# Kernel tuning notes

Measured on AMD Instinct MI355X. Metric: run time of the kernel, lower is better.

Reference implementation:

```python
import jax, jax.numpy as jnp
import numpy as np

HEADS = 8
HEAD_DIM = 64
INV_TEMP = HEAD_DIM ** -0.5
LN_EPS = 1e-5  # torch nn.LayerNorm default


def layer_norm(x, g, b):
    mu = jnp.mean(x, axis=-1, keepdims=True)
    var = jnp.var(x, axis=-1, keepdims=True)
    return (x - mu) * jax.lax.rsqrt(var + LN_EPS) * g + b


def setup_inputs() -> dict:
    key = jax.random.key(0)
    ks = jax.random.split(key, 10)
    B, P, N, C = 2, 64, 256, 512
    std = C ** -0.5
    return {
        "q": jax.random.normal(ks[0], (B, P, N, C), jnp.float32),
        "k": jax.random.normal(ks[1], (B, P, N, C), jnp.float32),
        "v": jax.random.normal(ks[2], (B, P, N, C), jnp.float32),
        "mask": jax.random.uniform(ks[3], (B, P, 1, N, N), jnp.float32),
        "pos_scores": jax.random.normal(ks[4], (1, 1, HEADS, N, N), jnp.float32),
        "ln_q_g": jnp.ones((C,), jnp.float32), "ln_q_b": jnp.zeros((C,), jnp.float32),
        "ln_k_g": jnp.ones((C,), jnp.float32), "ln_k_b": jnp.zeros((C,), jnp.float32),
        "ln_v_g": jnp.ones((C,), jnp.float32), "ln_v_b": jnp.zeros((C,), jnp.float32),
        "Wq": jax.random.normal(ks[5], (C, C), jnp.float32) * std,
        "Wk": jax.random.normal(ks[6], (C, C), jnp.float32) * std,
        "Wv": jax.random.normal(ks[7], (C, C), jnp.float32) * std,
        "Wo": jax.random.normal(ks[8], (C, C), jnp.float32) * std,
        "bo": jnp.zeros((C,), jnp.float32),
    }


def reference(q, k, v, mask, pos_scores, ln_q_g, ln_q_b, ln_k_g, ln_k_b,
              ln_v_g, ln_v_b, Wq, Wk, Wv, Wo, bo):
    B, P, N, C = q.shape
    # pre-norm + projections (nn.Linear: y = x @ W^T)
    qh = jnp.einsum('bpnc,ec->bpne', layer_norm(q, ln_q_g, ln_q_b), Wq)
    kh = jnp.einsum('bpnc,ec->bpne', layer_norm(k, ln_k_g, ln_k_b), Wk)
    vh = jnp.einsum('bpnc,ec->bpne', layer_norm(v, ln_v_g, ln_v_b), Wv)
    # split heads: b p n (h d) -> b p h n d
    split = lambda t: t.reshape(B, P, N, HEADS, HEAD_DIM).transpose(0, 1, 3, 2, 4)
    qh, kh, vh = split(qh), split(kh), split(vh)
    # windowed attention with additive pos bias and multiplicative mask
    sim = jnp.einsum('bphid,bphjd->bphij', qh, kh) * INV_TEMP
    sim = mask * (sim + pos_scores)
    attn = jax.nn.softmax(sim, axis=-1)
    out = jnp.einsum('bphij,bphjd->bphid', attn, vh)
    # merge heads: b p h n d -> b p n (h d)
    out = out.transpose(0, 1, 3, 2, 4).reshape(B, P, N, C)
    return jnp.einsum('bpnc,ec->bpne', out, Wo) + bo
```

## Files before the change

### kernel.cpp

```cpp
#include <hip/hip_runtime.h>
#include <hip/hip_fp16.h>

#define BP   128
#define NTOK 256
#define CDIM 512
#define ROWS 32768
#define NH   8
#define DH   64

typedef _Float16 h2_t __attribute__((ext_vector_type(2)));
typedef _Float16 h4_t __attribute__((ext_vector_type(4)));
typedef _Float16 h8_t __attribute__((ext_vector_type(8)));
typedef float    f4_t __attribute__((ext_vector_type(4)));
typedef unsigned int u2v __attribute__((ext_vector_type(2)));

__device__ __forceinline__ unsigned pkrtz(float a, float b) {
    return __builtin_bit_cast(unsigned, __builtin_amdgcn_cvt_pkrtz(a, b));
}

__device__ __forceinline__ void async16(const void* gptr, void* lptr) {
    __builtin_amdgcn_global_load_lds(
        (const __attribute__((address_space(1))) unsigned int*)gptr,
        (__attribute__((address_space(3))) unsigned int*)lptr, 16, 0, 0);
}

__device__ __forceinline__ u2v pl32swap(unsigned a, unsigned b) {
#if __has_builtin(__builtin_amdgcn_permlane32_swap)
    return __builtin_amdgcn_permlane32_swap(a, b, false, false);
#else
    const bool hi = (threadIdx.x & 32) != 0;
    unsigned sa = (unsigned)__shfl_xor((int)a, 32);
    unsigned sb = (unsigned)__shfl_xor((int)b, 32);
    u2v r; r[0] = hi ? sb : a; r[1] = hi ? b : sa; return r;
#endif
}

__device__ __forceinline__ u2v pl16swap(unsigned a, unsigned b) {
#if __has_builtin(__builtin_amdgcn_permlane16_swap)
    return __builtin_amdgcn_permlane16_swap(a, b, false, false);
#else
    const bool odd = (threadIdx.x & 16) != 0;
    unsigned sa = (unsigned)__shfl_xor((int)a, 16);
    unsigned sb = (unsigned)__shfl_xor((int)b, 16);
    u2v r; r[0] = odd ? sb : a; r[1] = odd ? b : sa; return r;
#endif
}

__global__ __launch_bounds__(256) void ln_cast(const float* __restrict__ x,
                                               const float* __restrict__ g,
                                               const float* __restrict__ b,
                                               _Float16* __restrict__ y) {
    const int wave = threadIdx.x >> 6, lane = threadIdx.x & 63;
    const size_t row = (size_t)blockIdx.x * 4 + wave;
    const float4* xr = (const float4*)(x + row * CDIM);
    float4 a0 = xr[2 * lane], a1 = xr[2 * lane + 1];
    float s  = a0.x + a0.y + a0.z + a0.w + a1.x + a1.y + a1.z + a1.w;
    float ss = a0.x * a0.x + a0.y * a0.y + a0.z * a0.z + a0.w * a0.w +
               a1.x * a1.x + a1.y * a1.y + a1.z * a1.z + a1.w * a1.w;
#pragma unroll
    for (int off = 32; off; off >>= 1) {
        s  += __shfl_xor(s, off);
        ss += __shfl_xor(ss, off);
    }
    const float mu = s * (1.f / 512.f);
    const float rs = rsqrtf(ss * (1.f / 512.f) - mu * mu + 1e-5f);
    const float4* gp = (const float4*)g;
    const float4* bpp = (const float4*)b;
    float4 g0 = gp[2 * lane], g1 = gp[2 * lane + 1];
    float4 b0 = bpp[2 * lane], b1 = bpp[2 * lane + 1];
    h8_t o;
    o[0] = (_Float16)((a0.x - mu) * rs * g0.x + b0.x);
    o[1] = (_Float16)((a0.y - mu) * rs * g0.y + b0.y);
    o[2] = (_Float16)((a0.z - mu) * rs * g0.z + b0.z);
    o[3] = (_Float16)((a0.w - mu) * rs * g0.w + b0.w);
    o[4] = (_Float16)((a1.x - mu) * rs * g1.x + b1.x);
    o[5] = (_Float16)((a1.y - mu) * rs * g1.y + b1.y);
    o[6] = (_Float16)((a1.z - mu) * rs * g1.z + b1.z);
    o[7] = (_Float16)((a1.w - mu) * rs * g1.w + b1.w);
    ((h8_t*)(y + row * CDIM))[lane] = o;
}

__global__ __launch_bounds__(256) void cast_w4(const float* __restrict__ w0,
                                               const float* __restrict__ w1,
                                               const float* __restrict__ w2,
                                               const float* __restrict__ w3,
                                               _Float16* __restrict__ o) {
    const float* srcs[4] = {w0, w1, w2, w3};
    const float* w = srcs[blockIdx.y];
    const float scale = (blockIdx.y == 0) ? 0.125f : 1.0f;
    _Float16* dst = o + (size_t)blockIdx.y * (CDIM * CDIM);
    const int idx = blockIdx.x * 256 + threadIdx.x;
    float4 v = ((const float4*)w)[idx];
    h4_t ov = {(_Float16)(v.x * scale), (_Float16)(v.y * scale),
               (_Float16)(v.z * scale), (_Float16)(v.w * scale)};
    ((h4_t*)dst)[idx] = ov;
}

template <int MODE>
__global__ __launch_bounds__(256) void gemm_bt(const _Float16* __restrict__ A,
                                               const _Float16* __restrict__ Bw,
                                               _Float16* __restrict__ Ch,
                                               float* __restrict__ Cf,
                                               const float* __restrict__ bias) {
    constexpr int K = CDIM;
    __shared__ __align__(16) _Float16 As[128 * 64];
    __shared__ __align__(16) _Float16 Bs[128 * 64];
    const int t = threadIdx.x;
    const int wave = t >> 6, lane = t & 63;
    const int wm = wave & 1, wn = wave >> 1;

    const int bid = blockIdx.x;
    const int xcd = bid & 7, idx = bid >> 3;
    const size_t rowBase = (size_t)(xcd * 32 + (idx >> 2)) * 128;
    const int colBase = (idx & 3) * 128;

    f4_t acc[4][4] = {};

    const int srow = t >> 3;
    const int scol = (t & 7) * 8;
    const _Float16* Ap = A + (rowBase + srow) * K + scol;
    const _Float16* Bp = Bw + ((size_t)colBase + srow) * K + scol;
    char* AsB = (char*)As + wave * 1024;
    char* BsB = (char*)Bs + wave * 1024;

    for (int k0 = 0; k0 < K; k0 += 64) {
#pragma unroll
        for (int c = 0; c < 4; ++c) {
            async16(Ap + (size_t)(32 * c) * K + k0, AsB + c * 4096);
            async16(Bp + (size_t)(32 * c) * K + k0, BsB + c * 4096);
        }
        __syncthreads();
#pragma unroll
        for (int kk = 0; kk < 64; kk += 32) {
            h8_t af[4], bf[4];
#pragma unroll
            for (int i = 0; i < 4; ++i)
                af[i] = *(const h8_t*)(As + (wm * 64 + i * 16 + (lane & 15)) * 64 +
                                       kk + (lane >> 4) * 8);
#pragma unroll
            for (int j = 0; j < 4; ++j)
                bf[j] = *(const h8_t*)(Bs + (wn * 64 + j * 16 + (lane & 15)) * 64 +
                                       kk + (lane >> 4) * 8);
#pragma unroll
            for (int i = 0; i < 4; ++i)
#pragma unroll
                for (int j = 0; j < 4; ++j)
                    acc[i][j] = __builtin_amdgcn_mfma_f32_16x16x32_f16(
                        af[i], bf[j], acc[i][j], 0, 0, 0);
        }
        __syncthreads();
    }
#pragma unroll
    for (int i = 0; i < 4; ++i) {
        const size_t growb = rowBase + wm * 64 + i * 16 + ((lane >> 4) * 4);
#pragma unroll
        for (int j = 0; j < 4; ++j) {
            const int gcol = colBase + wn * 64 + j * 16 + (lane & 15);
            if (MODE == 2) {
                const int bp = (int)(growb >> 8), tok = (int)(growb & 255);
                const int hh = gcol >> 6, dd = gcol & 63;
                h4_t w = {(_Float16)acc[i][j][0], (_Float16)acc[i][j][1],
                          (_Float16)acc[i][j][2], (_Float16)acc[i][j][3]};
                *(h4_t*)(Ch + ((size_t)(bp * NH + hh) * DH + dd) * NTOK + tok) = w;
            } else {
#pragma unroll
                for (int r = 0; r < 4; ++r) {
                    const size_t idx2 = (growb + r) * CDIM + gcol;
                    if (MODE == 0)
                        Ch[idx2] = (_Float16)acc[i][j][r];
                    else
                        Cf[idx2] = acc[i][j][r] + bias[gcol];
                }
            }
        }
    }
}

__global__ __launch_bounds__(256, 2) void attn_mfma(const _Float16* __restrict__ Q,
                                                    const _Float16* __restrict__ K,
                                                    const _Float16* __restrict__ VT,
                                                    const float* __restrict__ mask,
                                                    const float* __restrict__ pos,
                                                    _Float16* __restrict__ O) {
    const int bid = blockIdx.x;
    const int xcd = bid & 7, idx = bid >> 3;
    const int bp = xcd + 8 * (idx >> 4);
    const int sub = idx & 15;
    const int h = sub & 7, qh = sub >> 3;

    const int t = threadIdx.x;
    const int wave = t >> 6, lane = t & 63;
    const int g = lane >> 4, li = lane & 15;

    __shared__ __align__(16) _Float16 Ks[2][64 * 64];
    __shared__ __align__(16) _Float16 VTs[2][64 * 64];

    const int i0 = qh * 128 + wave * 32;

    h8_t qf[2][2];
#pragma unroll
    for (int it = 0; it < 2; ++it)
#pragma unroll
        for (int x = 0; x < 2; ++x)
            qf[it][x] = *(const h8_t*)(Q +
                (size_t)(bp * NTOK + i0 + it * 16 + li) * CDIM +
                h * DH + x * 32 + g * 8);

    const int srow = wave * 16 + (lane >> 3);
    const int sslot = (lane & 7) ^ ((lane >> 3) & 7);
    const _Float16* kSrc = K + ((size_t)(bp * NTOK) + srow) * CDIM + h * DH + sslot * 8;
    const _Float16* vSrc = VT + ((size_t)((bp * NH + h) * DH) + srow) * NTOK + sslot * 8;
    char* KsB[2] = {(char*)Ks[0] + wave * 2048, (char*)Ks[1] + wave * 2048};
    char* VsB[2] = {(char*)VTs[0] + wave * 2048, (char*)VTs[1] + wave * 2048};

    const int sw = li & 7;
    const int cx0 = (g ^ sw) * 8;
    const int cx1 = ((4 + g) ^ sw) * 8;

    const float* mrow0 = mask + (size_t)bp * (NTOK * NTOK) + (size_t)(i0 + li) * NTOK + g * 4;
    const float* prow0 = pos + (size_t)h * (NTOK * NTOK) + (size_t)(i0 + li) * NTOK + g * 4;

    f4_t o[4][2] = {};
    float lp[2] = {0.f, 0.f};

    async16(kSrc, KsB[0]);
    async16(kSrc + 8 * CDIM, KsB[0] + 1024);
    async16(vSrc, VsB[0]);
    async16(vSrc + 8 * NTOK, VsB[0] + 1024);

#pragma unroll
    for (int c = 0; c < 4; ++c) {
        const int cur = c & 1;
        if (c < 3) {
            const int nb = cur ^ 1;
            async16(kSrc + (size_t)(c + 1) * 64 * CDIM, KsB[nb]);
            async16(kSrc + (size_t)(c + 1) * 64 * CDIM + 8 * CDIM, KsB[nb] + 1024);
            async16(vSrc + (c + 1) * 64, VsB[nb]);
            async16(vSrc + (c + 1) * 64 + 8 * NTOK, VsB[nb] + 1024);
            asm volatile("s_waitcnt vmcnt(4)" ::: "memory");
        } else {
            asm volatile("s_waitcnt vmcnt(0)" ::: "memory");
        }
        __builtin_amdgcn_s_barrier();
        __builtin_amdgcn_sched_barrier(0);

        const _Float16* Kc = Ks[cur];
        const _Float16* Vc = VTs[cur];

        f4_t s[4][2] = {};
#pragma unroll
        for (int x = 0; x < 2; ++x) {
            const int cc = x ? cx1 : cx0;
            h8_t kf[4];
#pragma unroll
            for (int jt = 0; jt < 4; ++jt)
                kf[jt] = *(const h8_t*)(Kc + (jt * 16 + li) * 64 + cc);
#pragma unroll
            for (int jt = 0; jt < 4; ++jt)
#pragma unroll
                for (int it = 0; it < 2; ++it)
                    s[jt][it] = __builtin_amdgcn_mfma_f32_16x16x32_f16(
                        kf[jt], qf[it][x], s[jt][it], 0, 0, 0);
        }

        h8_t pf[2][2];
#pragma unroll
        for (int it = 0; it < 2; ++it) {
            const float* mr = mrow0 + it * (16 * NTOK) + c * 64;
            const float* pr = prow0 + it * (16 * NTOK) + c * 64;
            unsigned pk[4][2];
#pragma unroll
            for (int jt = 0; jt < 4; ++jt) {
                float4 mm = *(const float4*)(mr + jt * 16);
                float4 pp = *(const float4*)(pr + jt * 16);
                float e0 = __expf((s[jt][it][0] + pp.x) * mm.x);
                float e1 = __expf((s[jt][it][1] + pp.y) * mm.y);
                float e2 = __expf((s[jt][it][2] + pp.z) * mm.z);
                float e3 = __expf((s[jt][it][3] + pp.w) * mm.w);
                lp[it] += (e0 + e1) + (e2 + e3);
                pk[jt][0] = pkrtz(e0, e1);
                pk[jt][1] = pkrtz(e2, e3);
            }
#pragma unroll
            for (int x = 0; x < 2; ++x) {
                u2v r0 = pl32swap(pk[2 * x][0], pk[2 * x + 1][0]);
                u2v r1 = pl32swap(pk[2 * x][1], pk[2 * x + 1][1]);
                u2v q0 = pl16swap(r0[0], r0[1]);
                u2v q1 = pl16swap(r1[0], r1[1]);
                union { unsigned u[4]; h8_t v; } u;
                u.u[0] = q0[0]; u.u[1] = q1[0]; u.u[2] = q0[1]; u.u[3] = q1[1];
                pf[it][x] = u.v;
            }
        }

#pragma unroll
        for (int x = 0; x < 2; ++x) {
            const int cc = x ? cx1 : cx0;
            h8_t vf[4];
#pragma unroll
            for (int dt = 0; dt < 4; ++dt)
                vf[dt] = *(const h8_t*)(Vc + (dt * 16 + li) * 64 + cc);
#pragma unroll
            for (int dt = 0; dt < 4; ++dt)
#pragma unroll
                for (int it = 0; it < 2; ++it)
                    o[dt][it] = __builtin_amdgcn_mfma_f32_16x16x32_f16(
                        vf[dt], pf[it][x], o[dt][it], 0, 0, 0);
        }
        __builtin_amdgcn_sched_barrier(0);
        __builtin_amdgcn_s_barrier();
    }

    float inv[2];
#pragma unroll
    for (int it = 0; it < 2; ++it) {
        float l = lp[it];
        l += __shfl_xor(l, 16);
        l += __shfl_xor(l, 32);
        inv[it] = __builtin_amdgcn_rcpf(l);
    }
#pragma unroll
    for (int dt = 0; dt < 4; ++dt)
#pragma unroll
        for (int it = 0; it < 2; ++it) {
            const int i = i0 + it * 16 + li;
            h4_t w = {(_Float16)(o[dt][it][0] * inv[it]),
                      (_Float16)(o[dt][it][1] * inv[it]),
                      (_Float16)(o[dt][it][2] * inv[it]),
                      (_Float16)(o[dt][it][3] * inv[it])};
            *(h4_t*)(O + (size_t)(bp * NTOK + i) * CDIM + h * DH + dt * 16 +
                     g * 4) = w;
        }
}

extern "C" void kernel_launch(void* const* d_in, const int* in_sizes, int n_in,
                              void* d_out, int out_size, void* d_ws, size_t ws_size,
                              hipStream_t stream) {
    const float* q    = (const float*)d_in[0];
    const float* k    = (const float*)d_in[1];
    const float* v    = (const float*)d_in[2];
    const float* mask = (const float*)d_in[3];
    const float* pos  = (const float*)d_in[4];
    const float* lnqg = (const float*)d_in[5];
    const float* lnqb = (const float*)d_in[6];
    const float* lnkg = (const float*)d_in[7];
    const float* lnkb = (const float*)d_in[8];
    const float* lnvg = (const float*)d_in[9];
    const float* lnvb = (const float*)d_in[10];
    const float* Wq   = (const float*)d_in[11];
    const float* Wk   = (const float*)d_in[12];
    const float* Wv   = (const float*)d_in[13];
    const float* Wo   = (const float*)d_in[14];
    const float* bo   = (const float*)d_in[15];
    float* out = (float*)d_out;

    char* ws = (char*)d_ws;
    const size_t XSZ = (size_t)ROWS * CDIM * sizeof(_Float16);
    _Float16* XB  = (_Float16*)ws;
    _Float16* WH  = (_Float16*)(ws + XSZ);
    _Float16* QHp = (_Float16*)(ws + XSZ + 4 * (size_t)(CDIM * CDIM) * sizeof(_Float16));
    _Float16* KHp = QHp + (size_t)ROWS * CDIM;
    _Float16* VTg = KHp + (size_t)ROWS * CDIM;

    cast_w4<<<dim3(256, 4), 256, 0, stream>>>(Wq, Wk, Wv, Wo, WH);

    ln_cast<<<8192, 256, 0, stream>>>(q, lnqg, lnqb, XB);
    gemm_bt<0><<<1024, 256, 0, stream>>>(XB, WH + 0 * (CDIM * CDIM), QHp, nullptr, nullptr);
    ln_cast<<<8192, 256, 0, stream>>>(k, lnkg, lnkb, XB);
    gemm_bt<0><<<1024, 256, 0, stream>>>(XB, WH + 1 * (CDIM * CDIM), KHp, nullptr, nullptr);
    ln_cast<<<8192, 256, 0, stream>>>(v, lnvg, lnvb, XB);
    gemm_bt<2><<<1024, 256, 0, stream>>>(XB, WH + 2 * (CDIM * CDIM), VTg, nullptr, nullptr);

    attn_mfma<<<2048, 256, 0, stream>>>(QHp, KHp, VTg, mask, pos, XB);

    gemm_bt<1><<<1024, 256, 0, stream>>>(XB, WH + 3 * (CDIM * CDIM), nullptr, out, bo);
}
```

Baseline: 460.6 us.

## Load K and V fragments directly from global memory, drop LDS staging

Removes the double-buffered LDS staging of K and V^T tiles (async global-to-LDS copies, waitcnt and block barriers). Each wave now reads its MFMA operand fragments straight from global memory, relying on L1/L2 to serve the reuse across the four waves. This drops barrier synchronisation and LDS traffic and frees LDS for occupancy. In exchange it adds redundant global loads per wave and loses the explicit prefetch overlap, so the MFMAs may stall on memory latency.

```diff
diff --git a/kernel.cpp b/kernel.cpp
--- a/kernel.cpp
+++ b/kernel.cpp
@@ -192,9 +192,6 @@
     const int wave = t >> 6, lane = t & 63;
     const int g = lane >> 4, li = lane & 15;
 
-    __shared__ __align__(16) _Float16 Ks[2][64 * 64];
-    __shared__ __align__(16) _Float16 VTs[2][64 * 64];
-
     const int i0 = qh * 128 + wave * 32;
 
     h8_t qf[2][2];
@@ -206,16 +203,8 @@
                 (size_t)(bp * NTOK + i0 + it * 16 + li) * CDIM +
                 h * DH + x * 32 + g * 8);
 
-    const int srow = wave * 16 + (lane >> 3);
-    const int sslot = (lane & 7) ^ ((lane >> 3) & 7);
-    const _Float16* kSrc = K + ((size_t)(bp * NTOK) + srow) * CDIM + h * DH + sslot * 8;
-    const _Float16* vSrc = VT + ((size_t)((bp * NH + h) * DH) + srow) * NTOK + sslot * 8;
-    char* KsB[2] = {(char*)Ks[0] + wave * 2048, (char*)Ks[1] + wave * 2048};
-    char* VsB[2] = {(char*)VTs[0] + wave * 2048, (char*)VTs[1] + wave * 2048};
-
-    const int sw = li & 7;
-    const int cx0 = (g ^ sw) * 8;
-    const int cx1 = ((4 + g) ^ sw) * 8;
+    const _Float16* Kb = K + ((size_t)(bp * NTOK) + li) * CDIM + h * DH + g * 8;
+    const _Float16* Vb = VT + ((size_t)((bp * NH + h) * DH) + li) * NTOK + g * 8;
 
     const float* mrow0 = mask + (size_t)bp * (NTOK * NTOK) + (size_t)(i0 + li) * NTOK + g * 4;
     const float* prow0 = pos + (size_t)h * (NTOK * NTOK) + (size_t)(i0 + li) * NTOK + g * 4;
@@ -223,38 +212,16 @@
     f4_t o[4][2] = {};
     float lp[2] = {0.f, 0.f};
 
-    async16(kSrc, KsB[0]);
-    async16(kSrc + 8 * CDIM, KsB[0] + 1024);
-    async16(vSrc, VsB[0]);
-    async16(vSrc + 8 * NTOK, VsB[0] + 1024);
-
 #pragma unroll
     for (int c = 0; c < 4; ++c) {
-        const int cur = c & 1;
-        if (c < 3) {
-            const int nb = cur ^ 1;
-            async16(kSrc + (size_t)(c + 1) * 64 * CDIM, KsB[nb]);
-            async16(kSrc + (size_t)(c + 1) * 64 * CDIM + 8 * CDIM, KsB[nb] + 1024);
-            async16(vSrc + (c + 1) * 64, VsB[nb]);
-            async16(vSrc + (c + 1) * 64 + 8 * NTOK, VsB[nb] + 1024);
-            asm volatile("s_waitcnt vmcnt(4)" ::: "memory");
-        } else {
-            asm volatile("s_waitcnt vmcnt(0)" ::: "memory");
-        }
-        __builtin_amdgcn_s_barrier();
-        __builtin_amdgcn_sched_barrier(0);
-
-        const _Float16* Kc = Ks[cur];
-        const _Float16* Vc = VTs[cur];
-
         f4_t s[4][2] = {};
 #pragma unroll
         for (int x = 0; x < 2; ++x) {
-            const int cc = x ? cx1 : cx0;
             h8_t kf[4];
 #pragma unroll
             for (int jt = 0; jt < 4; ++jt)
-                kf[jt] = *(const h8_t*)(Kc + (jt * 16 + li) * 64 + cc);
+                kf[jt] = *(const h8_t*)(Kb + (size_t)(c * 64 + jt * 16) * CDIM +
+                                        x * 32);
 #pragma unroll
             for (int jt = 0; jt < 4; ++jt)
 #pragma unroll
@@ -295,11 +262,11 @@
 
 #pragma unroll
         for (int x = 0; x < 2; ++x) {
-            const int cc = x ? cx1 : cx0;
             h8_t vf[4];
 #pragma unroll
             for (int dt = 0; dt < 4; ++dt)
-                vf[dt] = *(const h8_t*)(Vc + (dt * 16 + li) * 64 + cc);
+                vf[dt] = *(const h8_t*)(Vb + (size_t)(dt * 16) * NTOK +
+                                        c * 64 + x * 32);
 #pragma unroll
             for (int dt = 0; dt < 4; ++dt)
 #pragma unroll
@@ -307,8 +274,6 @@
                     o[dt][it] = __builtin_amdgcn_mfma_f32_16x16x32_f16(
                         vf[dt], pf[it][x], o[dt][it], 0, 0, 0);
         }
-        __builtin_amdgcn_sched_barrier(0);
-        __builtin_amdgcn_s_barrier();
     }
 
     float inv[2];
```

New measurement: 514.6 us. +11.7%, slower.
